# Kernel tuning notes

Measured on AMD Instinct MI355X. Metric: run time of the kernel, lower is better.

Reference implementation:

```python
import jax, jax.numpy as jnp
import numpy as np

N = 10000      # num nodes
D = 256        # embedding dim (in_channels)
Q = 4096       # num query edges
P = 0.003      # edge density (~30 avg degree)


def setup_inputs() -> dict:
    key = jax.random.key(0)
    k1, k2, k3 = jax.random.split(key, 3)
    emb_weight = jax.random.normal(k1, (N, D), dtype=jnp.float32)
    # 0/1 dense adjacency standing in for the SparseTensor adj
    adj = (jax.random.uniform(k2, (N, N)) < P).astype(jnp.float32)
    edges = jax.random.randint(k3, (2, Q), 0, N, dtype=jnp.int64)
    return {"emb_weight": emb_weight, "adj": adj, "edges": edges}


def reference(emb_weight, adj, edges):
    # model_type='simplecos', x=None -> x = emb.weight
    x = emb_weight
    degrees = adj.sum(-1) + 1e-6                      # [N]
    # x = x + (adj @ x) / degrees[:, None]  (torch precedence: matmul then div)
    x = x + (adj @ x) / degrees[:, None]              # [N, D]
    # cosine_similarity with eps=1e-8 (torch default)
    nrm = jnp.sqrt(jnp.sum(x * x, axis=1))            # [N]
    xn = x / jnp.maximum(nrm, 1e-8)[:, None]          # [N, D]
    # common neighbors: elementwise product of adjacency rows of the two endpoints
    src, dst = edges[0], edges[1]
    cn = adj[src] * adj[dst]                          # [Q, N]
    mask = (cn != 0).astype(x.dtype)                  # [Q, N] indicator of common neighbor
    # cos(x[src[e]], x[c]) and cos(x[dst[e]], x[c]) for every candidate neighbor c
    cosL = xn[src] @ xn.T                             # [Q, N]
    cosR = xn[dst] @ xn.T                             # [Q, N]
    # sparse segment-sum over common-neighbor columns
    weights = jnp.sum(mask * cosL * cosR, axis=1)     # [Q]
    return jax.nn.sigmoid(weights)
```

## Files before the change

kernel.cpp:

```cpp
#include <hip/hip_runtime.h>
#include <math.h>

#define NN 10000
#define DD 256
#define QQ 4096
#define CAP 128

typedef float  fx4 __attribute__((ext_vector_type(4)));


__global__ __launch_bounds__(256) void scan_rows(
    const float* __restrict__ adj, int* __restrict__ cnt, int* __restrict__ nbr)
{
    const int lane = threadIdx.x & 63;
    const int wid  = (blockIdx.x << 2) | (threadIdx.x >> 6);
    const int nw   = gridDim.x << 2;
    const unsigned long long lmask = (1ull << lane) - 1ull;

    for (int row = wid; row < NN; row += nw) {
        const fx4* rp  = (const fx4*)(adj + (size_t)row * NN);
        int* outp = nbr + (size_t)row * CAP;
        int base = 0;

        fx4 b0 = __builtin_nontemporal_load(&rp[lane]);
        fx4 b1 = __builtin_nontemporal_load(&rp[64  + lane]);
        fx4 b2 = __builtin_nontemporal_load(&rp[128 + lane]);
        fx4 b3 = __builtin_nontemporal_load(&rp[192 + lane]);

        #define CKCOMP(val, col)                                                  \
            { unsigned long long _b = __ballot((val) != 0.f);                     \
              if ((val) != 0.f) {                                                 \
                  int _p = base + (int)__popcll(_b & lmask);                      \
                  if (_p < CAP) outp[_p] = (col);                                 \
              }                                                                   \
              base += (int)__popcll(_b); }

        #define CKCHUNK(v, cidx)                                                  \
            { int _cb = (cidx) * 256 + lane * 4;                                  \
              CKCOMP(v.x, _cb); CKCOMP(v.y, _cb + 1);                             \
              CKCOMP(v.z, _cb + 2); CKCOMP(v.w, _cb + 3); }

        for (int cc = 0; cc < 40; cc += 4) {
            fx4 v0 = b0, v1 = b1, v2 = b2, v3 = b3;
            int n0 = (cc + 4) * 64 + lane;
            int n1 = (cc + 5) * 64 + lane;
            int n2 = (cc + 6) * 64 + lane;
            int n3 = (cc + 7) * 64 + lane;
            b0 = (n0 < 2500) ? __builtin_nontemporal_load(&rp[n0]) : (fx4){0.f,0.f,0.f,0.f};
            b1 = (n1 < 2500) ? __builtin_nontemporal_load(&rp[n1]) : (fx4){0.f,0.f,0.f,0.f};
            b2 = (n2 < 2500) ? __builtin_nontemporal_load(&rp[n2]) : (fx4){0.f,0.f,0.f,0.f};
            b3 = (n3 < 2500) ? __builtin_nontemporal_load(&rp[n3]) : (fx4){0.f,0.f,0.f,0.f};
            CKCHUNK(v0, cc);
            CKCHUNK(v1, cc + 1);
            CKCHUNK(v2, cc + 2);
            CKCHUNK(v3, cc + 3);
        }
        #undef CKCHUNK
        #undef CKCOMP

        if (lane == 0) cnt[row] = base;
    }
}

__global__ __launch_bounds__(256) void gather_rows(
    const float* __restrict__ emb, const int* __restrict__ cnt,
    const int* __restrict__ nbr, float* __restrict__ xn)
{
    const int i = blockIdx.x;
    const int t = threadIdx.x;
    __shared__ int   s_list[CAP];
    __shared__ float s_red[4];
    __shared__ float s_norm;

    const int c = cnt[i];
    const int m = (c < CAP) ? c : CAP;

    const float self = emb[(size_t)i * DD + t];
    if (t < m) s_list[t] = nbr[(size_t)i * CAP + t];
    __syncthreads();

    float a0=0.f,a1=0.f,a2=0.f,a3=0.f,a4=0.f,a5=0.f,a6=0.f,a7=0.f;
    int k = 0;
    for (; k + 8 <= m; k += 8) {
        int i0=s_list[k],   i1=s_list[k+1], i2=s_list[k+2], i3=s_list[k+3];
        int i4=s_list[k+4], i5=s_list[k+5], i6=s_list[k+6], i7=s_list[k+7];
        a0 += emb[(size_t)i0*DD + t]; a1 += emb[(size_t)i1*DD + t];
        a2 += emb[(size_t)i2*DD + t]; a3 += emb[(size_t)i3*DD + t];
        a4 += emb[(size_t)i4*DD + t]; a5 += emb[(size_t)i5*DD + t];
        a6 += emb[(size_t)i6*DD + t]; a7 += emb[(size_t)i7*DD + t];
    }
    for (; k < m; ++k) a0 += emb[(size_t)s_list[k]*DD + t];
    const float acc = ((a0+a1)+(a2+a3)) + ((a4+a5)+(a6+a7));

    const float deg = (float)c + 1e-6f;
    const float x = self + acc / deg;

    float s = x * x;
    #pragma unroll
    for (int o = 32; o > 0; o >>= 1) s += __shfl_down(s, o, 64);
    const int lane = t & 63, wv = t >> 6;
    if (lane == 0) s_red[wv] = s;
    __syncthreads();
    if (t == 0) {
        float tot = s_red[0] + s_red[1] + s_red[2] + s_red[3];
        s_norm = fmaxf(sqrtf(tot), 1e-8f);
    }
    __syncthreads();

    xn[(size_t)i * DD + t] = x / s_norm;
}

__global__ __launch_bounds__(64) void edge_weights(
    const int* __restrict__ edges, const float* __restrict__ xn,
    const int* __restrict__ cnt, const int* __restrict__ nbr,
    float* __restrict__ out)
{
    const int e = blockIdx.x;
    const int lane = threadIdx.x;
    const int srcI = edges[e];
    const int dstI = edges[QQ + e];

    __shared__ int s_dst[CAP];
    __shared__ int s_com[CAP];
    __shared__ int s_ncom;

    const int2 sA = ((const int2*)(nbr + (size_t)srcI * CAP))[lane];
    const int2 dA = ((const int2*)(nbr + (size_t)dstI * CAP))[lane];
    const int cs0 = cnt[srcI];
    const int cd0 = cnt[dstI];
    const int cs = (cs0 < CAP) ? cs0 : CAP;
    const int cd = (cd0 < CAP) ? cd0 : CAP;

    if (lane == 0) s_ncom = 0;
    s_dst[2 * lane]     = dA.x;
    s_dst[2 * lane + 1] = dA.y;
    __syncthreads();

    {
        int k0 = 2 * lane, k1 = 2 * lane + 1;
        if (k0 < cs) {
            bool f = false;
            for (int j = 0; j < cd; ++j) { if (s_dst[j] == sA.x) { f = true; break; } }
            if (f) { int p = atomicAdd(&s_ncom, 1); s_com[p] = sA.x; }
        }
        if (k1 < cs) {
            bool f = false;
            for (int j = 0; j < cd; ++j) { if (s_dst[j] == sA.y) { f = true; break; } }
            if (f) { int p = atomicAdd(&s_ncom, 1); s_com[p] = sA.y; }
        }
    }
    __syncthreads();

    const int nc = s_ncom;
    if (nc == 0) { if (lane == 0) out[e] = 0.5f; return; }

    const float4 vs = ((const float4*)(xn + (size_t)srcI * DD))[lane];
    const float4 vd = ((const float4*)(xn + (size_t)dstI * DD))[lane];

    float w = 0.f;
    for (int q = 0; q < nc; ++q) {
        const float4 vc = ((const float4*)(xn + (size_t)s_com[q] * DD))[lane];
        float a = vs.x*vc.x + vs.y*vc.y + vs.z*vc.z + vs.w*vc.w;
        float b = vd.x*vc.x + vd.y*vc.y + vd.z*vc.z + vd.w*vc.w;
        #pragma unroll
        for (int o = 32; o > 0; o >>= 1) {
            a += __shfl_xor(a, o, 64);
            b += __shfl_xor(b, o, 64);
        }
        w += a * b;
    }
    if (lane == 0) out[e] = 1.f / (1.f + expf(-w));
}

extern "C" void kernel_launch(void* const* d_in, const int* in_sizes, int n_in,
                              void* d_out, int out_size, void* d_ws, size_t ws_size,
                              hipStream_t stream) {
    const float* emb   = (const float*)d_in[0];
    const float* adj   = (const float*)d_in[1];
    const int*   edges = (const int*)d_in[2];
    float*       out   = (float*)d_out;

    float* xn  = (float*)d_ws;
    int*   cnt = (int*)(xn + (size_t)NN * DD);
    int*   nbr = cnt + NN;

    scan_rows<<<1024, 256, 0, stream>>>(adj, cnt, nbr);
    gather_rows<<<NN, 256, 0, stream>>>(emb, cnt, nbr, xn);
    edge_weights<<<QQ, 64, 0, stream>>>(edges, xn, cnt, nbr, out);
}
```

Baseline: 537.4 us.

## Fuse scan, gather and edge kernels into one cooperative persistent kernel

```diff
diff --git a/kernel.cpp b/kernel.cpp
--- a/kernel.cpp
+++ b/kernel.cpp
@@ -1,13 +1,179 @@
 #include <hip/hip_runtime.h>
+#include <hip/hip_cooperative_groups.h>
 #include <math.h>
+
+namespace cg = cooperative_groups;
 
 #define NN 10000
 #define DD 256
 #define QQ 4096
 #define CAP 128
+#define NB 1024
 
 typedef float  fx4 __attribute__((ext_vector_type(4)));
 
+
+__global__ __launch_bounds__(256) void fused(
+    const float* __restrict__ emb, const float* __restrict__ adj,
+    const int* __restrict__ edges, float* __restrict__ out,
+    float* __restrict__ xn, int* __restrict__ cnt, int* __restrict__ nbr)
+{
+    cg::grid_group grid = cg::this_grid();
+    const int t    = threadIdx.x;
+    const int lane = t & 63;
+    const int wv   = t >> 6;
+
+    __shared__ int   s_list[CAP];
+    __shared__ float s_red[4];
+    __shared__ float s_norm;
+    __shared__ int   s_dst[4][CAP];
+    __shared__ int   s_com[4][CAP];
+    __shared__ int   s_nc[4];
+
+    {
+        const int wid = (blockIdx.x << 2) | wv;
+        const unsigned long long lmask = (1ull << lane) - 1ull;
+
+        for (int row = wid; row < NN; row += (NB << 2)) {
+            const fx4* rp  = (const fx4*)(adj + (size_t)row * NN);
+            int* outp = nbr + (size_t)row * CAP;
+            int base = 0;
+
+            fx4 b0 = __builtin_nontemporal_load(&rp[lane]);
+            fx4 b1 = __builtin_nontemporal_load(&rp[64  + lane]);
+            fx4 b2 = __builtin_nontemporal_load(&rp[128 + lane]);
+            fx4 b3 = __builtin_nontemporal_load(&rp[192 + lane]);
+
+            #define CKCOMP(val, col)                                              \
+                { unsigned long long _b = __ballot((val) != 0.f);                 \
+                  if ((val) != 0.f) {                                             \
+                      int _p = base + (int)__popcll(_b & lmask);                  \
+                      if (_p < CAP) outp[_p] = (col);                             \
+                  }                                                               \
+                  base += (int)__popcll(_b); }
+
+            #define CKCHUNK(v, cidx)                                              \
+                { int _cb = (cidx) * 256 + lane * 4;                              \
+                  CKCOMP(v.x, _cb); CKCOMP(v.y, _cb + 1);                         \
+                  CKCOMP(v.z, _cb + 2); CKCOMP(v.w, _cb + 3); }
+
+            for (int cc = 0; cc < 40; cc += 4) {
+                fx4 v0 = b0, v1 = b1, v2 = b2, v3 = b3;
+                int n0 = (cc + 4) * 64 + lane;
+                int n1 = (cc + 5) * 64 + lane;
+                int n2 = (cc + 6) * 64 + lane;
+                int n3 = (cc + 7) * 64 + lane;
+                b0 = (n0 < 2500) ? __builtin_nontemporal_load(&rp[n0]) : (fx4){0.f,0.f,0.f,0.f};
+                b1 = (n1 < 2500) ? __builtin_nontemporal_load(&rp[n1]) : (fx4){0.f,0.f,0.f,0.f};
+                b2 = (n2 < 2500) ? __builtin_nontemporal_load(&rp[n2]) : (fx4){0.f,0.f,0.f,0.f};
+                b3 = (n3 < 2500) ? __builtin_nontemporal_load(&rp[n3]) : (fx4){0.f,0.f,0.f,0.f};
+                CKCHUNK(v0, cc);
+                CKCHUNK(v1, cc + 1);
+                CKCHUNK(v2, cc + 2);
+                CKCHUNK(v3, cc + 3);
+            }
+            #undef CKCHUNK
+            #undef CKCOMP
+
+            if (lane == 0) cnt[row] = base;
+        }
+    }
+    __threadfence();
+    grid.sync();
+
+    for (int i = blockIdx.x; i < NN; i += NB) {
+        const int c = cnt[i];
+        const int m = (c < CAP) ? c : CAP;
+
+        const float self = emb[(size_t)i * DD + t];
+        if (t < m) s_list[t] = nbr[(size_t)i * CAP + t];
+        __syncthreads();
+
+        float a0=0.f,a1=0.f,a2=0.f,a3=0.f,a4=0.f,a5=0.f,a6=0.f,a7=0.f;
+        int k = 0;
+        for (; k + 8 <= m; k += 8) {
+            int i0=s_list[k],   i1=s_list[k+1], i2=s_list[k+2], i3=s_list[k+3];
+            int i4=s_list[k+4], i5=s_list[k+5], i6=s_list[k+6], i7=s_list[k+7];
+            a0 += emb[(size_t)i0*DD + t]; a1 += emb[(size_t)i1*DD + t];
+            a2 += emb[(size_t)i2*DD + t]; a3 += emb[(size_t)i3*DD + t];
+            a4 += emb[(size_t)i4*DD + t]; a5 += emb[(size_t)i5*DD + t];
+            a6 += emb[(size_t)i6*DD + t]; a7 += emb[(size_t)i7*DD + t];
+        }
+        for (; k < m; ++k) a0 += emb[(size_t)s_list[k]*DD + t];
+        const float acc = ((a0+a1)+(a2+a3)) + ((a4+a5)+(a6+a7));
+
+        const float deg = (float)c + 1e-6f;
+        const float x = self + acc / deg;
+
+        float s = x * x;
+        #pragma unroll
+        for (int o = 32; o > 0; o >>= 1) s += __shfl_down(s, o, 64);
+        if (lane == 0) s_red[wv] = s;
+        __syncthreads();
+        if (t == 0) {
+            float tot = s_red[0] + s_red[1] + s_red[2] + s_red[3];
+            s_norm = fmaxf(sqrtf(tot), 1e-8f);
+        }
+        __syncthreads();
+
+        xn[(size_t)i * DD + t] = x / s_norm;
+        __syncthreads();
+    }
+    __threadfence();
+    grid.sync();
+
+    {
+        const int e = (blockIdx.x << 2) | wv;
+        const int srcI = edges[e];
+        const int dstI = edges[QQ + e];
+
+        const int2 sA = ((const int2*)(nbr + (size_t)srcI * CAP))[lane];
+        const int2 dA = ((const int2*)(nbr + (size_t)dstI * CAP))[lane];
+        int cs = cnt[srcI]; cs = (cs < CAP) ? cs : CAP;
+        int cd = cnt[dstI]; cd = (cd < CAP) ? cd : CAP;
+
+        if (lane == 0) s_nc[wv] = 0;
+        s_dst[wv][2 * lane]     = dA.x;
+        s_dst[wv][2 * lane + 1] = dA.y;
+        __syncthreads();
+
+        {
+            int k0 = 2 * lane, k1 = 2 * lane + 1;
+            if (k0 < cs) {
+                bool f = false;
+                for (int j = 0; j < cd; ++j) { if (s_dst[wv][j] == sA.x) { f = true; break; } }
+                if (f) { int p = atomicAdd(&s_nc[wv], 1); s_com[wv][p] = sA.x; }
+            }
+            if (k1 < cs) {
+                bool f = false;
+                for (int j = 0; j < cd; ++j) { if (s_dst[wv][j] == sA.y) { f = true; break; } }
+                if (f) { int p = atomicAdd(&s_nc[wv], 1); s_com[wv][p] = sA.y; }
+            }
+        }
+        __syncthreads();
+
+        const int nc = s_nc[wv];
+        if (nc == 0) {
+            if (lane == 0) out[e] = 0.5f;
+        } else {
+            const float4 vs = ((const float4*)(xn + (size_t)srcI * DD))[lane];
+            const float4 vd = ((const float4*)(xn + (size_t)dstI * DD))[lane];
+            float w = 0.f;
+            for (int q = 0; q < nc; ++q) {
+                const float4 vc = ((const float4*)(xn + (size_t)s_com[wv][q] * DD))[lane];
+                float a = vs.x*vc.x + vs.y*vc.y + vs.z*vc.z + vs.w*vc.w;
+                float b = vd.x*vc.x + vd.y*vc.y + vd.z*vc.z + vd.w*vc.w;
+                #pragma unroll
+                for (int o = 32; o > 0; o >>= 1) {
+                    a += __shfl_xor(a, o, 64);
+                    b += __shfl_xor(b, o, 64);
+                }
+                w += a * b;
+            }
+            if (lane == 0) out[e] = 1.f / (1.f + expf(-w));
+        }
+    }
+}
 
 __global__ __launch_bounds__(256) void scan_rows(
     const float* __restrict__ adj, int* __restrict__ cnt, int* __restrict__ nbr)
@@ -98,8 +264,8 @@
     float s = x * x;
     #pragma unroll
     for (int o = 32; o > 0; o >>= 1) s += __shfl_down(s, o, 64);
-    const int lane = t & 63, wv = t >> 6;
-    if (lane == 0) s_red[wv] = s;
+    const int lane = t & 63, wvv = t >> 6;
+    if (lane == 0) s_red[wvv] = s;
     __syncthreads();
     if (t == 0) {
         float tot = s_red[0] + s_red[1] + s_red[2] + s_red[3];
@@ -184,7 +350,14 @@
     int*   cnt = (int*)(xn + (size_t)NN * DD);
     int*   nbr = cnt + NN;
 
-    scan_rows<<<1024, 256, 0, stream>>>(adj, cnt, nbr);
-    gather_rows<<<NN, 256, 0, stream>>>(emb, cnt, nbr, xn);
-    edge_weights<<<QQ, 64, 0, stream>>>(edges, xn, cnt, nbr, out);
-}
+    void* args[] = { (void*)&emb, (void*)&adj, (void*)&edges, (void*)&out,
+                     (void*)&xn, (void*)&cnt, (void*)&nbr };
+    hipError_t err = hipLaunchCooperativeKernel((const void*)fused,
+                                                dim3(NB), dim3(256),
+                                                args, 0, stream);
+    if (err != hipSuccess) {
+        scan_rows<<<1024, 256, 0, stream>>>(adj, cnt, nbr);
+        gather_rows<<<NN, 256, 0, stream>>>(emb, cnt, nbr, xn);
+        edge_weights<<<QQ, 64, 0, stream>>>(edges, xn, cnt, nbr, out);
+    }
+}
```

Result: slower. 1.051 ms (+95.5%).

## Fuse neighbor gather into adjacency scan, software-pipelined across rows

Applied to the files above, without the earlier changes.

```diff
diff --git a/kernel.cpp b/kernel.cpp
--- a/kernel.cpp
+++ b/kernel.cpp
@@ -9,13 +9,55 @@
 typedef float  fx4 __attribute__((ext_vector_type(4)));
 
 
-__global__ __launch_bounds__(256) void scan_rows(
-    const float* __restrict__ adj, int* __restrict__ cnt, int* __restrict__ nbr)
+__global__ __launch_bounds__(256) void scan_gather(
+    const float* __restrict__ adj, const float* __restrict__ emb,
+    int* __restrict__ cnt, int* __restrict__ nbr, float* __restrict__ xn)
 {
     const int lane = threadIdx.x & 63;
     const int wid  = (blockIdx.x << 2) | (threadIdx.x >> 6);
     const int nw   = gridDim.x << 2;
     const unsigned long long lmask = (1ull << lane) - 1ull;
+    const float4* E = (const float4*)emb;
+
+    int pv = 0, prow = 0, pc = 0, pm = 0, pj = 0;
+    int pmy0 = 0, pmy1 = 0;
+    float4 pself = {0.f, 0.f, 0.f, 0.f};
+    float ax = 0.f, ay = 0.f, az = 0.f, aw = 0.f;
+
+#define NIDX(J) __shfl(((J) < 64) ? pmy0 : pmy1, (J) & 63, 64)
+
+#define GFIN()                                                                \
+    {                                                                         \
+        for (; pj + 4 <= pm; pj += 4) {                                       \
+            const int i0 = NIDX(pj),     i1 = NIDX(pj + 1);                   \
+            const int i2 = NIDX(pj + 2), i3 = NIDX(pj + 3);                   \
+            float4 g0 = E[(size_t)i0 * 64 + lane];                            \
+            float4 g1 = E[(size_t)i1 * 64 + lane];                            \
+            float4 g2 = E[(size_t)i2 * 64 + lane];                            \
+            float4 g3 = E[(size_t)i3 * 64 + lane];                            \
+            ax += (g0.x + g1.x) + (g2.x + g3.x);                              \
+            ay += (g0.y + g1.y) + (g2.y + g3.y);                              \
+            az += (g0.z + g1.z) + (g2.z + g3.z);                              \
+            aw += (g0.w + g1.w) + (g2.w + g3.w);                              \
+        }                                                                     \
+        for (; pj < pm; ++pj) {                                               \
+            const int i0 = NIDX(pj);                                          \
+            float4 g0 = E[(size_t)i0 * 64 + lane];                            \
+            ax += g0.x; ay += g0.y; az += g0.z; aw += g0.w;                    \
+        }                                                                     \
+        const float deg = (float)pc + 1e-6f;                                  \
+        const float xx = pself.x + ax / deg;                                  \
+        const float xy = pself.y + ay / deg;                                  \
+        const float xz = pself.z + az / deg;                                  \
+        const float xw = pself.w + aw / deg;                                  \
+        float s = xx * xx + xy * xy + xz * xz + xw * xw;                      \
+        _Pragma("unroll")                                                     \
+        for (int o = 32; o > 0; o >>= 1) s += __shfl_xor(s, o, 64);           \
+        const float inv = 1.f / fmaxf(sqrtf(s), 1e-8f);                       \
+        float4 r4;                                                            \
+        r4.x = xx * inv; r4.y = xy * inv; r4.z = xz * inv; r4.w = xw * inv;   \
+        ((float4*)xn)[(size_t)prow * 64 + lane] = r4;                         \
+    }
 
     for (int row = wid; row < NN; row += nw) {
         const fx4* rp  = (const fx4*)(adj + (size_t)row * NN);
@@ -27,87 +69,70 @@
         fx4 b2 = __builtin_nontemporal_load(&rp[128 + lane]);
         fx4 b3 = __builtin_nontemporal_load(&rp[192 + lane]);
 
-        #define CKCOMP(val, col)                                                  \
-            { unsigned long long _b = __ballot((val) != 0.f);                     \
-              if ((val) != 0.f) {                                                 \
-                  int _p = base + (int)__popcll(_b & lmask);                      \
-                  if (_p < CAP) outp[_p] = (col);                                 \
-              }                                                                   \
-              base += (int)__popcll(_b); }
-
-        #define CKCHUNK(v, cidx)                                                  \
-            { int _cb = (cidx) * 256 + lane * 4;                                  \
-              CKCOMP(v.x, _cb); CKCOMP(v.y, _cb + 1);                             \
-              CKCOMP(v.z, _cb + 2); CKCOMP(v.w, _cb + 3); }
+#define CKCOMP(val, col)                                                      \
+        { unsigned long long _b = __ballot((val) != 0.f);                     \
+          if ((val) != 0.f) {                                                 \
+              int _p = base + (int)__popcll(_b & lmask);                      \
+              if (_p < CAP) outp[_p] = (col);                                 \
+          }                                                                   \
+          base += (int)__popcll(_b); }
+
+#define CKCHUNK(v, cidx)                                                      \
+        { int _cb = (cidx) * 256 + lane * 4;                                  \
+          CKCOMP(v.x, _cb); CKCOMP(v.y, _cb + 1);                             \
+          CKCOMP(v.z, _cb + 2); CKCOMP(v.w, _cb + 3); }
 
         for (int cc = 0; cc < 40; cc += 4) {
             fx4 v0 = b0, v1 = b1, v2 = b2, v3 = b3;
-            int n0 = (cc + 4) * 64 + lane;
-            int n1 = (cc + 5) * 64 + lane;
-            int n2 = (cc + 6) * 64 + lane;
-            int n3 = (cc + 7) * 64 + lane;
+
+            const bool  gact = (pv != 0) && (pj + 4 <= pm);
+            const float gw   = gact ? 1.f : 0.f;
+            const int   jj   = gact ? pj : 0;
+            const int i0 = NIDX(jj),     i1 = NIDX(jj + 1);
+            const int i2 = NIDX(jj + 2), i3 = NIDX(jj + 3);
+            float4 g0 = E[(size_t)i0 * 64 + lane];
+            float4 g1 = E[(size_t)i1 * 64 + lane];
+            float4 g2 = E[(size_t)i2 * 64 + lane];
+            float4 g3 = E[(size_t)i3 * 64 + lane];
+
+            const int n0 = (cc + 4) * 64 + lane;
+            const int n1 = (cc + 5) * 64 + lane;
+            const int n2 = (cc + 6) * 64 + lane;
+            const int n3 = (cc + 7) * 64 + lane;
             b0 = (n0 < 2500) ? __builtin_nontemporal_load(&rp[n0]) : (fx4){0.f,0.f,0.f,0.f};
             b1 = (n1 < 2500) ? __builtin_nontemporal_load(&rp[n1]) : (fx4){0.f,0.f,0.f,0.f};
             b2 = (n2 < 2500) ? __builtin_nontemporal_load(&rp[n2]) : (fx4){0.f,0.f,0.f,0.f};
             b3 = (n3 < 2500) ? __builtin_nontemporal_load(&rp[n3]) : (fx4){0.f,0.f,0.f,0.f};
+
             CKCHUNK(v0, cc);
             CKCHUNK(v1, cc + 1);
             CKCHUNK(v2, cc + 2);
             CKCHUNK(v3, cc + 3);
-        }
-        #undef CKCHUNK
-        #undef CKCOMP
+
+            ax = fmaf(gw, (g0.x + g1.x) + (g2.x + g3.x), ax);
+            ay = fmaf(gw, (g0.y + g1.y) + (g2.y + g3.y), ay);
+            az = fmaf(gw, (g0.z + g1.z) + (g2.z + g3.z), az);
+            aw = fmaf(gw, (g0.w + g1.w) + (g2.w + g3.w), aw);
+            pj += gact ? 4 : 0;
+        }
+#undef CKCHUNK
+#undef CKCOMP
+
+        if (pv) GFIN();
 
         if (lane == 0) cnt[row] = base;
-    }
-}
-
-__global__ __launch_bounds__(256) void gather_rows(
-    const float* __restrict__ emb, const int* __restrict__ cnt,
-    const int* __restrict__ nbr, float* __restrict__ xn)
-{
-    const int i = blockIdx.x;
-    const int t = threadIdx.x;
-    __shared__ int   s_list[CAP];
-    __shared__ float s_red[4];
-    __shared__ float s_norm;
-
-    const int c = cnt[i];
-    const int m = (c < CAP) ? c : CAP;
-
-    const float self = emb[(size_t)i * DD + t];
-    if (t < m) s_list[t] = nbr[(size_t)i * CAP + t];
-    __syncthreads();
-
-    float a0=0.f,a1=0.f,a2=0.f,a3=0.f,a4=0.f,a5=0.f,a6=0.f,a7=0.f;
-    int k = 0;
-    for (; k + 8 <= m; k += 8) {
-        int i0=s_list[k],   i1=s_list[k+1], i2=s_list[k+2], i3=s_list[k+3];
-        int i4=s_list[k+4], i5=s_list[k+5], i6=s_list[k+6], i7=s_list[k+7];
-        a0 += emb[(size_t)i0*DD + t]; a1 += emb[(size_t)i1*DD + t];
-        a2 += emb[(size_t)i2*DD + t]; a3 += emb[(size_t)i3*DD + t];
-        a4 += emb[(size_t)i4*DD + t]; a5 += emb[(size_t)i5*DD + t];
-        a6 += emb[(size_t)i6*DD + t]; a7 += emb[(size_t)i7*DD + t];
-    }
-    for (; k < m; ++k) a0 += emb[(size_t)s_list[k]*DD + t];
-    const float acc = ((a0+a1)+(a2+a3)) + ((a4+a5)+(a6+a7));
-
-    const float deg = (float)c + 1e-6f;
-    const float x = self + acc / deg;
-
-    float s = x * x;
-    #pragma unroll
-    for (int o = 32; o > 0; o >>= 1) s += __shfl_down(s, o, 64);
-    const int lane = t & 63, wv = t >> 6;
-    if (lane == 0) s_red[wv] = s;
-    __syncthreads();
-    if (t == 0) {
-        float tot = s_red[0] + s_red[1] + s_red[2] + s_red[3];
-        s_norm = fmaxf(sqrtf(tot), 1e-8f);
-    }
-    __syncthreads();
-
-    xn[(size_t)i * DD + t] = x / s_norm;
+        pv = 1; prow = row; pc = base;
+        pm = (base < CAP) ? base : CAP;
+        pj = 0;
+        pmy0 = (lane < pm)      ? outp[lane]      : 0;
+        pmy1 = (64 + lane < pm) ? outp[64 + lane] : 0;
+        pself = E[(size_t)row * 64 + lane];
+        ax = ay = az = aw = 0.f;
+    }
+
+    if (pv) GFIN();
+#undef GFIN
+#undef NIDX
 }
 
 __global__ __launch_bounds__(64) void edge_weights(
@@ -184,7 +209,6 @@
     int*   cnt = (int*)(xn + (size_t)NN * DD);
     int*   nbr = cnt + NN;
 
-    scan_rows<<<1024, 256, 0, stream>>>(adj, cnt, nbr);
-    gather_rows<<<NN, 256, 0, stream>>>(emb, cnt, nbr, xn);
+    scan_gather<<<1024, 256, 0, stream>>>(adj, emb, cnt, nbr, xn);
     edge_weights<<<QQ, 64, 0, stream>>>(edges, xn, cnt, nbr, out);
 }
```

New measurement: 534.7 us. About the same (-0.5%).
